# Kernel optimization log

Measured on AMD Instinct MI355X. Metric: run time of the kernel, lower is better.

Reference implementation:

```python
import jax, jax.numpy as jnp
import numpy as np

B, S, D, H = 16384, 5, 512, 8
HD = D // H


def setup_inputs() -> dict:
    key = jax.random.key(0)
    ks = jax.random.split(key, 6)
    scale = 1.0 / np.sqrt(D)
    x = jax.random.normal(ks[0], (B, S, D), dtype=jnp.float32)
    Wq = jax.random.normal(ks[1], (D, D), dtype=jnp.float32) * scale
    Wk = jax.random.normal(ks[2], (D, D), dtype=jnp.float32) * scale
    Wv = jax.random.normal(ks[3], (D, D), dtype=jnp.float32) * scale
    Wo = jax.random.normal(ks[4], (D, D), dtype=jnp.float32) * scale
    bq = jnp.zeros((D,), jnp.float32)
    bk = jnp.zeros((D,), jnp.float32)
    bv = jnp.zeros((D,), jnp.float32)
    bo = jnp.zeros((D,), jnp.float32)
    # bias_init = zeros(H,5,5); bias_init[0,:,-1] = 1.0
    prop_bias = jnp.zeros((H, S, S), jnp.float32).at[0, :, -1].set(1.0)
    return {"x": x, "Wq": Wq, "bq": bq, "Wk": Wk, "bk": bk,
            "Wv": Wv, "bv": bv, "Wo": Wo, "bo": bo, "prop_bias": prop_bias}


def reference(x, Wq, bq, Wk, bk, Wv, bv, Wo, bo, prop_bias):
    b, s, d = x.shape
    # projections (torch Linear with weight stored as [in, out] here)
    q = (x @ Wq + bq).reshape(b, s, H, HD).transpose(0, 2, 1, 3)  # [b,h,s,hd]
    k = (x @ Wk + bk).reshape(b, s, H, HD).transpose(0, 2, 1, 3)
    v = (x @ Wv + bv).reshape(b, s, H, HD).transpose(0, 2, 1, 3)
    scores = jnp.einsum('bhsd,bhtd->bhst', q, k) / jnp.sqrt(jnp.float32(HD))
    scores = scores + prop_bias[None]  # learned per-head additive bias
    attn = jax.nn.softmax(scores, axis=-1)  # dropout is identity at eval
    out = jnp.einsum('bhst,bhtd->bhsd', attn, v)
    out = out.transpose(0, 2, 1, 3).reshape(b, s, d)
    return out @ Wo + bo
```

## Files before the change

kernel.cpp:

```cpp
#include <hip/hip_runtime.h>

typedef __attribute__((ext_vector_type(4))) float f32x4;
typedef __attribute__((ext_vector_type(8))) short bf16x8;
typedef __attribute__((ext_vector_type(8))) unsigned short u16x8;

__device__ __forceinline__ unsigned short f2bf(float f) {
  unsigned int u = __float_as_uint(f);
  u += 0x7FFFu + ((u >> 16) & 1u);
  return (unsigned short)(u >> 16);
}
__device__ __forceinline__ float bf2f(unsigned short s) {
  return __uint_as_float(((unsigned int)s) << 16);
}

__device__ __forceinline__ void gll16(const void* g, void* l) {
  __builtin_amdgcn_global_load_lds((const __attribute__((address_space(1))) void*)g,
                                   (__attribute__((address_space(3))) void*)l, 16, 0, 0);
}

__global__ __launch_bounds__(256) void cvt_f32_bf16(const float* __restrict__ in,
                                                    unsigned short* __restrict__ out,
                                                    int n8) {
  int i = blockIdx.x * blockDim.x + threadIdx.x;
  int stride = gridDim.x * blockDim.x;
  for (; i < n8; i += stride) {
    const float4* p = (const float4*)in + (size_t)i * 2;
    float4 a = p[0], b = p[1];
    u16x8 r;
    r[0] = f2bf(a.x); r[1] = f2bf(a.y); r[2] = f2bf(a.z); r[3] = f2bf(a.w);
    r[4] = f2bf(b.x); r[5] = f2bf(b.y); r[6] = f2bf(b.z); r[7] = f2bf(b.w);
    *(u16x8*)(out + (size_t)i * 8) = r;
  }
}

__global__ __launch_bounds__(1024) void wtrans(const float* __restrict__ W,
                                               unsigned short* __restrict__ Wt) {
  __shared__ float t[32][33];
  const int k0 = blockIdx.x * 32, n0 = blockIdx.y * 32;
  t[threadIdx.y][threadIdx.x] = W[(size_t)(k0 + threadIdx.y) * 512 + n0 + threadIdx.x];
  __syncthreads();
  Wt[(size_t)(n0 + threadIdx.y) * 512 + k0 + threadIdx.x] = f2bf(t[threadIdx.x][threadIdx.y]);
}

template <typename OutT>
__global__ __launch_bounds__(256) void gemm_bt(const unsigned short* __restrict__ A,
                                               const unsigned short* __restrict__ Bt,
                                               const float* __restrict__ bias,
                                               OutT* __restrict__ C) {
  __shared__ unsigned short As[128 * 64];
  __shared__ unsigned short Bs[128 * 64];

  const int tid = threadIdx.x;
  const int lane = tid & 63;
  const int wid = tid >> 6;
  const int wr = wid >> 1;
  const int wc = wid & 1;
  const int u = lane & 15;
  const int g = lane >> 4;

  const int flat = blockIdx.x;
  const int tile = ((flat & 7) * 320) + (flat >> 3);
  const int m0 = (tile >> 2) * 128;
  const int n0 = (tile & 3) * 128;

  f32x4 acc[4][4] = {};

  int sr[4], sck[4];
#pragma unroll
  for (int o = 0; o < 4; ++o) {
    int ci = o * 256 + tid;
    sr[o] = ci >> 3;
    sck[o] = (ci & 7) ^ (sr[o] & 7);
  }

  for (int kt = 0; kt < 8; ++kt) {
    const int kb = kt * 64;
#pragma unroll
    for (int o = 0; o < 4; ++o) {
      int ci = o * 256 + tid;
      gll16(A + (size_t)(m0 + sr[o]) * 512 + kb + sck[o] * 8, As + ci * 8);
    }
#pragma unroll
    for (int o = 0; o < 4; ++o) {
      int ci = o * 256 + tid;
      gll16(Bt + (size_t)(n0 + sr[o]) * 512 + kb + sck[o] * 8, Bs + ci * 8);
    }
    __syncthreads();
#pragma unroll
    for (int kk = 0; kk < 2; ++kk) {
      bf16x8 af[4], bfr[4];
#pragma unroll
      for (int mf = 0; mf < 4; ++mf) {
        int r = wr * 64 + mf * 16 + u;
        int slot = (kk * 4 + g) ^ (r & 7);
        af[mf] = *(const bf16x8*)(As + r * 64 + slot * 8);
      }
#pragma unroll
      for (int nf = 0; nf < 4; ++nf) {
        int r = wc * 64 + nf * 16 + u;
        int slot = (kk * 4 + g) ^ (r & 7);
        bfr[nf] = *(const bf16x8*)(Bs + r * 64 + slot * 8);
      }
#pragma unroll
      for (int mf = 0; mf < 4; ++mf)
#pragma unroll
        for (int nf = 0; nf < 4; ++nf)
          acc[mf][nf] = __builtin_amdgcn_mfma_f32_16x16x32_bf16(af[mf], bfr[nf], acc[mf][nf], 0, 0, 0);
    }
    __syncthreads();
  }

#pragma unroll
  for (int nf = 0; nf < 4; ++nf) {
    const int col = n0 + wc * 64 + nf * 16 + u;
    const float bv = bias[col];
#pragma unroll
    for (int mf = 0; mf < 4; ++mf) {
      const int rbase = m0 + wr * 64 + mf * 16 + 4 * g;
#pragma unroll
      for (int j = 0; j < 4; ++j) {
        float v = acc[mf][nf][j] + bv;
        if constexpr (sizeof(OutT) == 2) {
          ((unsigned short*)C)[(size_t)(rbase + j) * 512 + col] = f2bf(v);
        } else {
          ((float*)C)[(size_t)(rbase + j) * 512 + col] = v;
        }
      }
    }
  }
}

__global__ __launch_bounds__(256) void attn_s5(const unsigned short* __restrict__ qb,
                                               const unsigned short* __restrict__ kb,
                                               const unsigned short* __restrict__ vb,
                                               const float* __restrict__ pbias,
                                               unsigned short* __restrict__ ob) {
  __shared__ float sb[200];
  if (threadIdx.x < 200) sb[threadIdx.x] = pbias[threadIdx.x];
  __syncthreads();

  const int lane = threadIdx.x & 63;
  const int p = lane >> 4, u = lane & 15;
  const int wv = blockIdx.x * (blockDim.x >> 6) + (threadIdx.x >> 6);
  const int nwv = gridDim.x * (blockDim.x >> 6);
  const int NPG = (16384 * 8) / 4;

  for (int pg = wv; pg < NPG; pg += nwv) {
    const int idx = pg * 4 + p;
    const int b = idx >> 3, h = idx & 7;
    const size_t base = (size_t)(b * 5) * 512 + h * 64 + u * 4;

    float qf[5][4], kf[5][4], vf[5][4];
#pragma unroll
    for (int s = 0; s < 5; ++s) {
      ushort4 tq = *(const ushort4*)(qb + base + (size_t)s * 512);
      ushort4 tk = *(const ushort4*)(kb + base + (size_t)s * 512);
      ushort4 tv = *(const ushort4*)(vb + base + (size_t)s * 512);
      qf[s][0] = bf2f(tq.x); qf[s][1] = bf2f(tq.y); qf[s][2] = bf2f(tq.z); qf[s][3] = bf2f(tq.w);
      kf[s][0] = bf2f(tk.x); kf[s][1] = bf2f(tk.y); kf[s][2] = bf2f(tk.z); kf[s][3] = bf2f(tk.w);
      vf[s][0] = bf2f(tv.x); vf[s][1] = bf2f(tv.y); vf[s][2] = bf2f(tv.z); vf[s][3] = bf2f(tv.w);
    }

    float sc[5][5];
#pragma unroll
    for (int s = 0; s < 5; ++s)
#pragma unroll
      for (int t = 0; t < 5; ++t)
        sc[s][t] = qf[s][0] * kf[t][0] + qf[s][1] * kf[t][1] + qf[s][2] * kf[t][2] + qf[s][3] * kf[t][3];

#pragma unroll
    for (int m = 1; m < 16; m <<= 1)
#pragma unroll
      for (int s = 0; s < 5; ++s)
#pragma unroll
        for (int t = 0; t < 5; ++t)
          sc[s][t] += __shfl_xor(sc[s][t], m, 64);

    const float* bh = &sb[h * 25];
#pragma unroll
    for (int s = 0; s < 5; ++s) {
      float r0 = sc[s][0] * 0.125f + bh[s * 5 + 0];
      float r1 = sc[s][1] * 0.125f + bh[s * 5 + 1];
      float r2 = sc[s][2] * 0.125f + bh[s * 5 + 2];
      float r3 = sc[s][3] * 0.125f + bh[s * 5 + 3];
      float r4 = sc[s][4] * 0.125f + bh[s * 5 + 4];
      float mx = fmaxf(fmaxf(fmaxf(r0, r1), fmaxf(r2, r3)), r4);
      float e0 = __expf(r0 - mx), e1 = __expf(r1 - mx), e2 = __expf(r2 - mx),
            e3 = __expf(r3 - mx), e4 = __expf(r4 - mx);
      float rd = 1.0f / (e0 + e1 + e2 + e3 + e4);
      ushort4 o;
      float o0, o1, o2, o3;
      o0 = (e0 * vf[0][0] + e1 * vf[1][0] + e2 * vf[2][0] + e3 * vf[3][0] + e4 * vf[4][0]) * rd;
      o1 = (e0 * vf[0][1] + e1 * vf[1][1] + e2 * vf[2][1] + e3 * vf[3][1] + e4 * vf[4][1]) * rd;
      o2 = (e0 * vf[0][2] + e1 * vf[1][2] + e2 * vf[2][2] + e3 * vf[3][2] + e4 * vf[4][2]) * rd;
      o3 = (e0 * vf[0][3] + e1 * vf[1][3] + e2 * vf[2][3] + e3 * vf[3][3] + e4 * vf[4][3]) * rd;
      o.x = f2bf(o0); o.y = f2bf(o1); o.z = f2bf(o2); o.w = f2bf(o3);
      *(ushort4*)(ob + base + (size_t)s * 512) = o;
    }
  }
}

extern "C" void kernel_launch(void* const* d_in, const int* in_sizes, int n_in,
                              void* d_out, int out_size, void* d_ws, size_t ws_size,
                              hipStream_t stream) {
  const float* x  = (const float*)d_in[0];
  const float* Wq = (const float*)d_in[1];
  const float* bq = (const float*)d_in[2];
  const float* Wk = (const float*)d_in[3];
  const float* bk = (const float*)d_in[4];
  const float* Wv = (const float*)d_in[5];
  const float* bv = (const float*)d_in[6];
  const float* Wo = (const float*)d_in[7];
  const float* bo = (const float*)d_in[8];
  const float* pb = (const float*)d_in[9];

  char* ws = (char*)d_ws;
  unsigned short* wt = (unsigned short*)ws;
  unsigned short* xb = (unsigned short*)(ws + 2097152);
  unsigned short* qb = (unsigned short*)(ws + 85983232);
  unsigned short* kbuf = (unsigned short*)(ws + 169869312);
  unsigned short* vbuf = (unsigned short*)(ws + 253755392);

  cvt_f32_bf16<<<2048, 256, 0, stream>>>(x, xb, 5242880);

  dim3 tb(32, 32), tg(16, 16);
  wtrans<<<tg, tb, 0, stream>>>(Wq, wt + 0 * 262144);
  wtrans<<<tg, tb, 0, stream>>>(Wk, wt + 1 * 262144);
  wtrans<<<tg, tb, 0, stream>>>(Wv, wt + 2 * 262144);
  wtrans<<<tg, tb, 0, stream>>>(Wo, wt + 3 * 262144);

  gemm_bt<unsigned short><<<2560, 256, 0, stream>>>(xb, wt + 0 * 262144, bq, qb);
  gemm_bt<unsigned short><<<2560, 256, 0, stream>>>(xb, wt + 1 * 262144, bk, kbuf);
  gemm_bt<unsigned short><<<2560, 256, 0, stream>>>(xb, wt + 2 * 262144, bv, vbuf);

  attn_s5<<<2048, 256, 0, stream>>>(qb, kbuf, vbuf, pb, xb);

  gemm_bt<float><<<2560, 256, 0, stream>>>(xb, wt + 3 * 262144, bo, (float*)d_out);
}
```

Measured before the change: 648.6 us.

## Fuse Q/K/V projections into one GEMM and double-buffer LDS staging

The three separate Q, K and V projection GEMMs become a single GEMM over a concatenated 512x1536 transposed weight with a concatenated bias, writing an interleaved QKV buffer that the attention kernel reads. The GEMM kernel now double-buffers its A and B LDS tiles, so the load of the next K-slice is issued before computing on the current one and global latency overlaps with MFMA work. The intent is fewer launches, one pass over the activations instead of three, and hidden load latency. In exchange, LDS use per block doubles (64KB), which can limit occupancy despite launch_bounds(256,2), and a small bias-concatenation kernel is added.

```diff
diff --git a/kernel.cpp b/kernel.cpp
--- a/kernel.cpp
+++ b/kernel.cpp
@@ -42,50 +42,59 @@
   Wt[(size_t)(n0 + threadIdx.y) * 512 + k0 + threadIdx.x] = f2bf(t[threadIdx.x][threadIdx.y]);
 }
 
+__global__ __launch_bounds__(256) void bcat_k(const float* __restrict__ bq,
+                                              const float* __restrict__ bk,
+                                              const float* __restrict__ bv,
+                                              float* __restrict__ bc) {
+  int i = blockIdx.x * 256 + threadIdx.x;
+  if (i < 1536) {
+    float v = (i < 512) ? bq[i] : (i < 1024 ? bk[i - 512] : bv[i - 1024]);
+    bc[i] = v;
+  }
+}
+
 template <typename OutT>
-__global__ __launch_bounds__(256) void gemm_bt(const unsigned short* __restrict__ A,
-                                               const unsigned short* __restrict__ Bt,
-                                               const float* __restrict__ bias,
-                                               OutT* __restrict__ C) {
-  __shared__ unsigned short As[128 * 64];
-  __shared__ unsigned short Bs[128 * 64];
+__global__ __launch_bounds__(256, 2) void gemm2p(const unsigned short* __restrict__ A,
+                                                 const unsigned short* __restrict__ Bt,
+                                                 const float* __restrict__ bias,
+                                                 OutT* __restrict__ C,
+                                                 int Ntl, int Ncols) {
+  __shared__ unsigned short As[2][128 * 64];
+  __shared__ unsigned short Bs[2][128 * 64];
 
   const int tid = threadIdx.x;
   const int lane = tid & 63;
   const int wid = tid >> 6;
-  const int wr = wid >> 1;
-  const int wc = wid & 1;
-  const int u = lane & 15;
-  const int g = lane >> 4;
-
+  const int wr = wid >> 1, wc = wid & 1;
+  const int u = lane & 15, g = lane >> 4;
+
+  const int chunk = gridDim.x >> 3;
   const int flat = blockIdx.x;
-  const int tile = ((flat & 7) * 320) + (flat >> 3);
-  const int m0 = (tile >> 2) * 128;
-  const int n0 = (tile & 3) * 128;
+  const int tile = (flat & 7) * chunk + (flat >> 3);
+  const int mt = tile / Ntl, nt = tile - mt * Ntl;
+  const int m0 = mt * 128, n0 = nt * 128;
+
+  const unsigned short* ap[4];
+  const unsigned short* bp[4];
+  int ldsoff[4];
+#pragma unroll
+  for (int o = 0; o < 4; ++o) {
+    int c = o * 256 + tid;
+    int r = c >> 3, s = (c & 7) ^ (r & 7);
+    ldsoff[o] = c * 8;
+    ap[o] = A + (size_t)(m0 + r) * 512 + s * 8;
+    bp[o] = Bt + (size_t)(n0 + r) * 512 + s * 8;
+  }
 
   f32x4 acc[4][4] = {};
 
-  int sr[4], sck[4];
-#pragma unroll
-  for (int o = 0; o < 4; ++o) {
-    int ci = o * 256 + tid;
-    sr[o] = ci >> 3;
-    sck[o] = (ci & 7) ^ (sr[o] & 7);
-  }
-
-  for (int kt = 0; kt < 8; ++kt) {
-    const int kb = kt * 64;
-#pragma unroll
-    for (int o = 0; o < 4; ++o) {
-      int ci = o * 256 + tid;
-      gll16(A + (size_t)(m0 + sr[o]) * 512 + kb + sck[o] * 8, As + ci * 8);
-    }
-#pragma unroll
-    for (int o = 0; o < 4; ++o) {
-      int ci = o * 256 + tid;
-      gll16(Bt + (size_t)(n0 + sr[o]) * 512 + kb + sck[o] * 8, Bs + ci * 8);
-    }
-    __syncthreads();
+  auto STAGE = [&](int buf, int kb) {
+#pragma unroll
+    for (int o = 0; o < 4; ++o) gll16(ap[o] + kb, &As[buf][ldsoff[o]]);
+#pragma unroll
+    for (int o = 0; o < 4; ++o) gll16(bp[o] + kb, &Bs[buf][ldsoff[o]]);
+  };
+  auto COMPUTE = [&](int buf) {
 #pragma unroll
     for (int kk = 0; kk < 2; ++kk) {
       bf16x8 af[4], bfr[4];
@@ -93,13 +102,13 @@
       for (int mf = 0; mf < 4; ++mf) {
         int r = wr * 64 + mf * 16 + u;
         int slot = (kk * 4 + g) ^ (r & 7);
-        af[mf] = *(const bf16x8*)(As + r * 64 + slot * 8);
+        af[mf] = *(const bf16x8*)(&As[buf][r * 64 + slot * 8]);
       }
 #pragma unroll
       for (int nf = 0; nf < 4; ++nf) {
         int r = wc * 64 + nf * 16 + u;
         int slot = (kk * 4 + g) ^ (r & 7);
-        bfr[nf] = *(const bf16x8*)(Bs + r * 64 + slot * 8);
+        bfr[nf] = *(const bf16x8*)(&Bs[buf][r * 64 + slot * 8]);
       }
 #pragma unroll
       for (int mf = 0; mf < 4; ++mf)
@@ -107,8 +116,17 @@
         for (int nf = 0; nf < 4; ++nf)
           acc[mf][nf] = __builtin_amdgcn_mfma_f32_16x16x32_bf16(af[mf], bfr[nf], acc[mf][nf], 0, 0, 0);
     }
+  };
+
+  STAGE(0, 0);
+  __syncthreads();
+#pragma unroll
+  for (int kt = 0; kt < 7; ++kt) {
+    STAGE((kt + 1) & 1, (kt + 1) * 64);
+    COMPUTE(kt & 1);
     __syncthreads();
   }
+  COMPUTE(1);
 
 #pragma unroll
   for (int nf = 0; nf < 4; ++nf) {
@@ -121,20 +139,18 @@
       for (int j = 0; j < 4; ++j) {
         float v = acc[mf][nf][j] + bv;
         if constexpr (sizeof(OutT) == 2) {
-          ((unsigned short*)C)[(size_t)(rbase + j) * 512 + col] = f2bf(v);
+          ((unsigned short*)C)[(size_t)(rbase + j) * Ncols + col] = f2bf(v);
         } else {
-          ((float*)C)[(size_t)(rbase + j) * 512 + col] = v;
+          ((float*)C)[(size_t)(rbase + j) * Ncols + col] = v;
         }
       }
     }
   }
 }
 
-__global__ __launch_bounds__(256) void attn_s5(const unsigned short* __restrict__ qb,
-                                               const unsigned short* __restrict__ kb,
-                                               const unsigned short* __restrict__ vb,
+__global__ __launch_bounds__(256) void attn_s5(const unsigned short* __restrict__ qkv,
                                                const float* __restrict__ pbias,
-                                               unsigned short* __restrict__ ob) {
+                                               unsigned short* __restrict__ ao) {
   __shared__ float sb[200];
   if (threadIdx.x < 200) sb[threadIdx.x] = pbias[threadIdx.x];
   __syncthreads();
@@ -148,14 +164,14 @@
   for (int pg = wv; pg < NPG; pg += nwv) {
     const int idx = pg * 4 + p;
     const int b = idx >> 3, h = idx & 7;
-    const size_t base = (size_t)(b * 5) * 512 + h * 64 + u * 4;
+    const size_t rbase = (size_t)(b * 5) * 1536 + h * 64 + u * 4;
 
     float qf[5][4], kf[5][4], vf[5][4];
 #pragma unroll
     for (int s = 0; s < 5; ++s) {
-      ushort4 tq = *(const ushort4*)(qb + base + (size_t)s * 512);
-      ushort4 tk = *(const ushort4*)(kb + base + (size_t)s * 512);
-      ushort4 tv = *(const ushort4*)(vb + base + (size_t)s * 512);
+      ushort4 tq = *(const ushort4*)(qkv + rbase + (size_t)s * 1536);
+      ushort4 tk = *(const ushort4*)(qkv + rbase + (size_t)s * 1536 + 512);
+      ushort4 tv = *(const ushort4*)(qkv + rbase + (size_t)s * 1536 + 1024);
       qf[s][0] = bf2f(tq.x); qf[s][1] = bf2f(tq.y); qf[s][2] = bf2f(tq.z); qf[s][3] = bf2f(tq.w);
       kf[s][0] = bf2f(tk.x); kf[s][1] = bf2f(tk.y); kf[s][2] = bf2f(tk.z); kf[s][3] = bf2f(tk.w);
       vf[s][0] = bf2f(tv.x); vf[s][1] = bf2f(tv.y); vf[s][2] = bf2f(tv.z); vf[s][3] = bf2f(tv.w);
@@ -188,14 +204,13 @@
       float e0 = __expf(r0 - mx), e1 = __expf(r1 - mx), e2 = __expf(r2 - mx),
             e3 = __expf(r3 - mx), e4 = __expf(r4 - mx);
       float rd = 1.0f / (e0 + e1 + e2 + e3 + e4);
+      float o0 = (e0 * vf[0][0] + e1 * vf[1][0] + e2 * vf[2][0] + e3 * vf[3][0] + e4 * vf[4][0]) * rd;
+      float o1 = (e0 * vf[0][1] + e1 * vf[1][1] + e2 * vf[2][1] + e3 * vf[3][1] + e4 * vf[4][1]) * rd;
+      float o2 = (e0 * vf[0][2] + e1 * vf[1][2] + e2 * vf[2][2] + e3 * vf[3][2] + e4 * vf[4][2]) * rd;
+      float o3 = (e0 * vf[0][3] + e1 * vf[1][3] + e2 * vf[2][3] + e3 * vf[3][3] + e4 * vf[4][3]) * rd;
       ushort4 o;
-      float o0, o1, o2, o3;
-      o0 = (e0 * vf[0][0] + e1 * vf[1][0] + e2 * vf[2][0] + e3 * vf[3][0] + e4 * vf[4][0]) * rd;
-      o1 = (e0 * vf[0][1] + e1 * vf[1][1] + e2 * vf[2][1] + e3 * vf[3][1] + e4 * vf[4][1]) * rd;
-      o2 = (e0 * vf[0][2] + e1 * vf[1][2] + e2 * vf[2][2] + e3 * vf[3][2] + e4 * vf[4][2]) * rd;
-      o3 = (e0 * vf[0][3] + e1 * vf[1][3] + e2 * vf[2][3] + e3 * vf[3][3] + e4 * vf[4][3]) * rd;
       o.x = f2bf(o0); o.y = f2bf(o1); o.z = f2bf(o2); o.w = f2bf(o3);
-      *(ushort4*)(ob + base + (size_t)s * 512) = o;
+      *(ushort4*)(ao + (size_t)(b * 5 + s) * 512 + h * 64 + u * 4) = o;
     }
   }
 }
@@ -215,25 +230,24 @@
   const float* pb = (const float*)d_in[9];
 
   char* ws = (char*)d_ws;
-  unsigned short* wt = (unsigned short*)ws;
-  unsigned short* xb = (unsigned short*)(ws + 2097152);
-  unsigned short* qb = (unsigned short*)(ws + 85983232);
-  unsigned short* kbuf = (unsigned short*)(ws + 169869312);
-  unsigned short* vbuf = (unsigned short*)(ws + 253755392);
+  unsigned short* wt_all = (unsigned short*)ws;
+  unsigned short* wtO    = (unsigned short*)(ws + 1572864);
+  float*          bc     = (float*)(ws + 2097152);
+  unsigned short* xb     = (unsigned short*)(ws + 2103296);
+  unsigned short* qkv    = (unsigned short*)(ws + 85989376);
 
   cvt_f32_bf16<<<2048, 256, 0, stream>>>(x, xb, 5242880);
 
   dim3 tb(32, 32), tg(16, 16);
-  wtrans<<<tg, tb, 0, stream>>>(Wq, wt + 0 * 262144);
-  wtrans<<<tg, tb, 0, stream>>>(Wk, wt + 1 * 262144);
-  wtrans<<<tg, tb, 0, stream>>>(Wv, wt + 2 * 262144);
-  wtrans<<<tg, tb, 0, stream>>>(Wo, wt + 3 * 262144);
-
-  gemm_bt<unsigned short><<<2560, 256, 0, stream>>>(xb, wt + 0 * 262144, bq, qb);
-  gemm_bt<unsigned short><<<2560, 256, 0, stream>>>(xb, wt + 1 * 262144, bk, kbuf);
-  gemm_bt<unsigned short><<<2560, 256, 0, stream>>>(xb, wt + 2 * 262144, bv, vbuf);
-
-  attn_s5<<<2048, 256, 0, stream>>>(qb, kbuf, vbuf, pb, xb);
-
-  gemm_bt<float><<<2560, 256, 0, stream>>>(xb, wt + 3 * 262144, bo, (float*)d_out);
-}
+  wtrans<<<tg, tb, 0, stream>>>(Wq, wt_all + 0 * 262144);
+  wtrans<<<tg, tb, 0, stream>>>(Wk, wt_all + 1 * 262144);
+  wtrans<<<tg, tb, 0, stream>>>(Wv, wt_all + 2 * 262144);
+  wtrans<<<tg, tb, 0, stream>>>(Wo, wtO);
+  bcat_k<<<6, 256, 0, stream>>>(bq, bk, bv, bc);
+
+  gemm2p<unsigned short><<<7680, 256, 0, stream>>>(xb, wt_all, bc, qkv, 12, 1536);
+
+  attn_s5<<<2048, 256, 0, stream>>>(qkv, pb, xb);
+
+  gemm2p<float><<<2560, 256, 0, stream>>>(xb, wtO, bo, (float*)d_out, 4, 512);
+}
```

Result: no change. 646.1 us (-0.4%).
